# Optimization experiments

Hardware: AMD Instinct MI355X
Metric: run time of the kernel (lower is better)

The kernel has to match this reference:

```python
import jax, jax.numpy as jnp
import numpy as np
from jax.scipy.special import logsumexp

N_ALPHA = 8192
N_BETA = 8192
N_LAYERS = 16


def setup_inputs() -> dict:
    key = jax.random.key(0)
    k1, k2, k3 = jax.random.split(key, 3)
    alpha = jax.random.uniform(k1, (N_ALPHA,), jnp.float32, 1e-3, 1.0)
    alpha = alpha / alpha.sum()
    beta = jax.random.uniform(k2, (N_BETA,), jnp.float32, 1e-3, 1.0)
    beta = beta / beta.sum()
    C = jax.random.uniform(k3, (N_ALPHA, N_BETA), jnp.float32, 0.0, 1.0)
    eps = jnp.float32(0.1)
    return {"alpha": alpha, "beta": beta, "C": C, "eps": eps}


def reference(alpha, beta, C, eps):
    # Log-domain Sinkhorn iterations (tol=None -> run all n_layers).
    log_alpha = jnp.log(alpha)
    log_beta = jnp.log(beta)

    def step(carry, _):
        _, g = carry
        # log_dot_exp(C, g, eps): logsumexp over n_beta axis of (-C + g[None,:]) / eps
        f = eps * (log_alpha - logsumexp((g[None, :] - C) / eps, axis=-1))
        # log_dot_exp(C.T, f, eps): logsumexp over n_alpha axis of (-C + f[:,None]) / eps
        g_new = eps * (log_beta - logsumexp((f[:, None] - C) / eps, axis=0))
        return (f, g_new), None

    init = (jnp.zeros_like(alpha), jnp.zeros_like(beta))
    (f, g), _ = jax.lax.scan(step, init, None, length=N_LAYERS)
    return f, g
```

## Files before the change

kernel.cpp:

```cpp
#include <hip/hip_runtime.h>

#define NA 8192
#define NB 8192
#define N_LAYERS 16

typedef _Float16 half_t;
typedef _Float16 half8_t __attribute__((ext_vector_type(8)));
typedef float float4_t __attribute__((ext_vector_type(4)));

__device__ __forceinline__ void barrier_lds() {
    asm volatile("s_waitcnt lgkmcnt(0)" ::: "memory");
    __builtin_amdgcn_s_barrier();
    asm volatile("" ::: "memory");
}

template <bool READ_C, bool WRITE_E, bool HAS_V>
__global__ __launch_bounds__(256, 2) void sink_fused(
    const float* __restrict__ C, const half_t* __restrict__ Ein,
    half_t* __restrict__ Eout, const float* __restrict__ v,
    const float* __restrict__ alpha, const float* __restrict__ d_eps,
    float* __restrict__ u, float* __restrict__ partial, int n_groups)
{
    const int t = threadIdx.x;
    const int rc = blockIdx.x;
    const int row0 = rc * (n_groups * 2);
    __shared__ float sred[2][8];

    float4_t w0[4], w1[4];
    if constexpr (HAS_V) {
        const float4_t* vv = (const float4_t*)v;
#pragma unroll
        for (int k = 0; k < 4; ++k) {
            const int g = k * 256 + t;
            w0[k] = vv[2 * g];
            w1[k] = vv[2 * g + 1];
        }
    }

    float acc[4][8];
#pragma unroll
    for (int k = 0; k < 4; ++k)
#pragma unroll
        for (int j = 0; j < 8; ++j) acc[k][j] = 0.0f;

    auto usum = [&](float rs0, float rs1, int par) -> float2 {
#pragma unroll
        for (int m = 1; m < 64; m <<= 1) {
            rs0 += __shfl_xor(rs0, m, 64);
            rs1 += __shfl_xor(rs1, m, 64);
        }
        const int lane = t & 63, wid = t >> 6;
        if (lane == 0) { sred[par][wid * 2] = rs0; sred[par][wid * 2 + 1] = rs1; }
        barrier_lds();
        const float S0 = (sred[par][0] + sred[par][2]) + (sred[par][4] + sred[par][6]);
        const float S1 = (sred[par][1] + sred[par][3]) + (sred[par][5] + sred[par][7]);
        return make_float2(S0, S1);
    };

    if constexpr (!READ_C) {
        const half8_t* Eb = (const half8_t*)Ein;
        half8_t bufA[2][4], bufB[2][4];

        auto load = [&](half8_t (&d)[2][4], int r0) {
#pragma unroll
            for (int rr = 0; rr < 2; ++rr)
#pragma unroll
                for (int k = 0; k < 4; ++k)
                    d[rr][k] = Eb[(size_t)(r0 + rr) * (NB / 8) + k * 256 + t];
        };

        auto step = [&](half8_t (&cur)[2][4], half8_t (&nxt)[2][4], int r0,
                        int par, bool pf) {
            if (pf) load(nxt, r0 + 2);
            const float a0 = alpha[r0], a1 = alpha[r0 + 1];
            float rs0 = 0.0f, rs1 = 0.0f;
#pragma unroll
            for (int k = 0; k < 4; ++k) {
                rs0 += (float)cur[0][k][0] * w0[k].x + (float)cur[0][k][1] * w0[k].y +
                       (float)cur[0][k][2] * w0[k].z + (float)cur[0][k][3] * w0[k].w +
                       (float)cur[0][k][4] * w1[k].x + (float)cur[0][k][5] * w1[k].y +
                       (float)cur[0][k][6] * w1[k].z + (float)cur[0][k][7] * w1[k].w;
                rs1 += (float)cur[1][k][0] * w0[k].x + (float)cur[1][k][1] * w0[k].y +
                       (float)cur[1][k][2] * w0[k].z + (float)cur[1][k][3] * w0[k].w +
                       (float)cur[1][k][4] * w1[k].x + (float)cur[1][k][5] * w1[k].y +
                       (float)cur[1][k][6] * w1[k].z + (float)cur[1][k][7] * w1[k].w;
            }
            const float2 S = usum(rs0, rs1, par);
            const float u0 = a0 / S.x, u1 = a1 / S.y;
            if (t == 0) { u[r0] = u0; u[r0 + 1] = u1; }
#pragma unroll
            for (int k = 0; k < 4; ++k)
#pragma unroll
                for (int j = 0; j < 8; ++j)
                    acc[k][j] += u0 * (float)cur[0][k][j] + u1 * (float)cur[1][k][j];
        };

        load(bufA, row0);
        for (int s = 0; s < n_groups; s += 2) {
            step(bufA, bufB, row0 + 2 * s, 0, true);
            step(bufB, bufA, row0 + 2 * (s + 1), 1, s + 2 < n_groups);
        }
    } else {
        const float inv_eps = 1.0f / d_eps[0];
        const float4_t* Cb = (const float4_t*)C;
        float4_t bufA[2][8], bufB[2][8];

        auto load = [&](float4_t (&d)[2][8], int r0) {
#pragma unroll
            for (int rr = 0; rr < 2; ++rr)
#pragma unroll
                for (int k = 0; k < 4; ++k) {
                    const int g = k * 256 + t;
                    d[rr][2 * k]     = Cb[(size_t)(r0 + rr) * (NB / 4) + 2 * g];
                    d[rr][2 * k + 1] = Cb[(size_t)(r0 + rr) * (NB / 4) + 2 * g + 1];
                }
        };

        auto step = [&](float4_t (&cur)[2][8], float4_t (&nxt)[2][8], int r0,
                        int par, bool pf) {
            if (pf) load(nxt, r0 + 2);
            const float a0 = alpha[r0], a1 = alpha[r0 + 1];
            half8_t h[2][4];
            float rs0 = 0.0f, rs1 = 0.0f;
#pragma unroll
            for (int rr = 0; rr < 2; ++rr) {
                float rs = 0.0f;
#pragma unroll
                for (int k = 0; k < 4; ++k) {
                    const float4_t c0 = cur[rr][2 * k], c1 = cur[rr][2 * k + 1];
                    const float e0 = __expf(-c0.x * inv_eps);
                    const float e1 = __expf(-c0.y * inv_eps);
                    const float e2 = __expf(-c0.z * inv_eps);
                    const float e3 = __expf(-c0.w * inv_eps);
                    const float e4 = __expf(-c1.x * inv_eps);
                    const float e5 = __expf(-c1.y * inv_eps);
                    const float e6 = __expf(-c1.z * inv_eps);
                    const float e7 = __expf(-c1.w * inv_eps);
                    h[rr][k][0] = (_Float16)e0; h[rr][k][1] = (_Float16)e1;
                    h[rr][k][2] = (_Float16)e2; h[rr][k][3] = (_Float16)e3;
                    h[rr][k][4] = (_Float16)e4; h[rr][k][5] = (_Float16)e5;
                    h[rr][k][6] = (_Float16)e6; h[rr][k][7] = (_Float16)e7;
                    if constexpr (HAS_V) {
                        rs += e0 * w0[k].x + e1 * w0[k].y + e2 * w0[k].z + e3 * w0[k].w +
                              e4 * w1[k].x + e5 * w1[k].y + e6 * w1[k].z + e7 * w1[k].w;
                    } else {
                        rs += ((e0 + e1) + (e2 + e3)) + ((e4 + e5) + (e6 + e7));
                    }
                }
                if (rr == 0) rs0 = rs; else rs1 = rs;
            }
            if constexpr (WRITE_E) {
#pragma unroll
                for (int rr = 0; rr < 2; ++rr)
#pragma unroll
                    for (int k = 0; k < 4; ++k)
                        ((half8_t*)Eout)[(size_t)(r0 + rr) * (NB / 8) + k * 256 + t] = h[rr][k];
            }
            const float2 S = usum(rs0, rs1, par);
            const float u0 = a0 / S.x, u1 = a1 / S.y;
            if (t == 0) { u[r0] = u0; u[r0 + 1] = u1; }
#pragma unroll
            for (int k = 0; k < 4; ++k)
#pragma unroll
                for (int j = 0; j < 8; ++j)
                    acc[k][j] += u0 * (float)h[0][k][j] + u1 * (float)h[1][k][j];
        };

        load(bufA, row0);
        for (int s = 0; s < n_groups; s += 2) {
            step(bufA, bufB, row0 + 2 * s, 0, true);
            step(bufB, bufA, row0 + 2 * (s + 1), 1, s + 2 < n_groups);
        }
    }

#pragma unroll
    for (int k = 0; k < 4; ++k) {
        float4_t o0 = {acc[k][0], acc[k][1], acc[k][2], acc[k][3]};
        float4_t o1 = {acc[k][4], acc[k][5], acc[k][6], acc[k][7]};
        float4_t* p = (float4_t*)(partial + (size_t)rc * NB + (size_t)(k * 256 + t) * 8);
        p[0] = o0;
        p[1] = o1;
    }
}

__global__ __launch_bounds__(256) void sink_v_combine(
    const float* __restrict__ partial, const float* __restrict__ beta,
    float* __restrict__ v, int nvc)
{
    const int c = blockIdx.x * 32 + (threadIdx.x & 31);
    const int sl = threadIdx.x >> 5;
    float s = 0.0f;
#pragma unroll 4
    for (int i = sl; i < nvc; i += 8) s += partial[(size_t)i * NB + c];
    __shared__ float sm[8][32];
    sm[sl][threadIdx.x & 31] = s;
    __syncthreads();
    if (threadIdx.x < 32) {
        float tot = 0.0f;
#pragma unroll
        for (int k = 0; k < 8; ++k) tot += sm[k][threadIdx.x];
        v[c] = beta[c] / tot;
    }
}

__global__ __launch_bounds__(256) void sink_finalize(
    const float* __restrict__ u, const float* __restrict__ v,
    const float* __restrict__ d_eps, float* __restrict__ out)
{
    const int i = blockIdx.x * 256 + threadIdx.x;
    const float eps = d_eps[0];
    if (i < NA) {
        out[i] = eps * logf(u[i]);
    } else if (i < NA + NB) {
        out[i] = eps * logf(v[i - NA]);
    }
}

extern "C" void kernel_launch(void* const* d_in, const int* in_sizes, int n_in,
                              void* d_out, int out_size, void* d_ws, size_t ws_size,
                              hipStream_t stream)
{
    const float* alpha = (const float*)d_in[0];
    const float* beta  = (const float*)d_in[1];
    const float* C     = (const float*)d_in[2];
    const float* d_eps = (const float*)d_in[3];
    float* out = (float*)d_out;

    const size_t eBytes   = (size_t)NA * NB * sizeof(half_t);
    const size_t vecBytes = (size_t)NA * sizeof(float);

    int nvc = 0;
    bool useE = false;
    if      (ws_size >= eBytes + (size_t)512 * NB * 4 + 2 * vecBytes) { useE = true; nvc = 512; }
    else if (ws_size >= eBytes + (size_t)256 * NB * 4 + 2 * vecBytes) { useE = true; nvc = 256; }
    else if (ws_size >= eBytes + (size_t)128 * NB * 4 + 2 * vecBytes) { useE = true; nvc = 128; }
    else if (ws_size >= (size_t)512 * NB * 4 + 2 * vecBytes)          { nvc = 512; }
    else if (ws_size >= (size_t)256 * NB * 4 + 2 * vecBytes)          { nvc = 256; }
    else                                                              { nvc = 128; }

    char* ws = (char*)d_ws;
    size_t off = 0;
    half_t* E = nullptr;
    if (useE) { E = (half_t*)ws; off += eBytes; }
    float* partial = (float*)(ws + off); off += (size_t)nvc * NB * sizeof(float);
    float* u = (float*)(ws + off); off += vecBytes;
    float* v = (float*)(ws + off);

    const int ng = (NA / nvc) / 2;
    const dim3 blk(256);
    const dim3 gridF(nvc);
    const dim3 gridC(NB / 32);
    const dim3 gridFin((NA + NB) / 256);

    for (int layer = 0; layer < N_LAYERS; ++layer) {
        if (layer == 0) {
            if (useE)
                sink_fused<true, true, false><<<gridF, blk, 0, stream>>>(
                    C, nullptr, E, nullptr, alpha, d_eps, u, partial, ng);
            else
                sink_fused<true, false, false><<<gridF, blk, 0, stream>>>(
                    C, nullptr, nullptr, nullptr, alpha, d_eps, u, partial, ng);
        } else {
            if (useE)
                sink_fused<false, false, true><<<gridF, blk, 0, stream>>>(
                    nullptr, E, nullptr, v, alpha, d_eps, u, partial, ng);
            else
                sink_fused<true, false, true><<<gridF, blk, 0, stream>>>(
                    C, nullptr, nullptr, v, alpha, d_eps, u, partial, ng);
        }
        sink_v_combine<<<gridC, blk, 0, stream>>>(partial, beta, v, nvc);
    }
    sink_finalize<<<gridFin, blk, 0, stream>>>(u, v, d_eps, out);
}
```

Baseline: 1.111 ms.

## Cache partial fp16 exp(-C/eps) rows and recompute the rest from C

Replaces the all-or-nothing fp16 E cache with a partial one: each block caches as many of its 16 rows as workspace allows and recomputes the remaining rows from C with exp. Blocks become 512 threads and always number 512, with separate layer-0 and later-layer kernels. This lets the E-cache path run when the workspace cannot hold the full matrix, at the cost of extra exp work and reading fp32 C for the uncached rows. The non-cached tail has no prefetch double-buffering.

```diff
diff --git a/kernel.cpp b/kernel.cpp
--- a/kernel.cpp
+++ b/kernel.cpp
@@ -3,6 +3,9 @@
 #define NA 8192
 #define NB 8192
 #define N_LAYERS 16
+#define RPB 16
+#define NBLK 512
+#define NTH 512
 
 typedef _Float16 half_t;
 typedef _Float16 half8_t __attribute__((ext_vector_type(8)));
@@ -14,34 +17,34 @@
     asm volatile("" ::: "memory");
 }
 
-template <bool READ_C, bool WRITE_E, bool HAS_V>
-__global__ __launch_bounds__(256, 2) void sink_fused(
-    const float* __restrict__ C, const half_t* __restrict__ Ein,
-    half_t* __restrict__ Eout, const float* __restrict__ v,
-    const float* __restrict__ alpha, const float* __restrict__ d_eps,
-    float* __restrict__ u, float* __restrict__ partial, int n_groups)
+__global__ __launch_bounds__(NTH, 4) void sink_fe(
+    const half_t* __restrict__ E, const float* __restrict__ C,
+    const float* __restrict__ v, const float* __restrict__ alpha,
+    const float* __restrict__ d_eps, float* __restrict__ u,
+    float* __restrict__ partial, int ngE)
 {
     const int t = threadIdx.x;
     const int rc = blockIdx.x;
-    const int row0 = rc * (n_groups * 2);
-    __shared__ float sred[2][8];
-
-    float4_t w0[4], w1[4];
-    if constexpr (HAS_V) {
-        const float4_t* vv = (const float4_t*)v;
-#pragma unroll
-        for (int k = 0; k < 4; ++k) {
-            const int g = k * 256 + t;
-            w0[k] = vv[2 * g];
-            w1[k] = vv[2 * g + 1];
-        }
-    }
-
-    float acc[4][8];
-#pragma unroll
-    for (int k = 0; k < 4; ++k)
+    const int row0 = rc * RPB;
+    __shared__ float sred[2][16];
+
+    const float4_t* vv = (const float4_t*)v;
+    float4_t w[4];
+#pragma unroll
+    for (int k = 0; k < 2; ++k) {
+        w[2 * k]     = vv[(size_t)(k * NTH + t) * 2];
+        w[2 * k + 1] = vv[(size_t)(k * NTH + t) * 2 + 1];
+    }
+
+    float acc[2][8];
+#pragma unroll
+    for (int k = 0; k < 2; ++k)
 #pragma unroll
         for (int j = 0; j < 8; ++j) acc[k][j] = 0.0f;
+
+    const half8_t* Eb = (const half8_t*)E + (size_t)rc * (2 * ngE) * (NB / 8);
+    const float4_t* Cb = (const float4_t*)C;
+    const float inv_eps = 1.0f / d_eps[0];
 
     auto usum = [&](float rs0, float rs1, int par) -> float2 {
 #pragma unroll
@@ -52,146 +55,231 @@
         const int lane = t & 63, wid = t >> 6;
         if (lane == 0) { sred[par][wid * 2] = rs0; sred[par][wid * 2 + 1] = rs1; }
         barrier_lds();
-        const float S0 = (sred[par][0] + sred[par][2]) + (sred[par][4] + sred[par][6]);
-        const float S1 = (sred[par][1] + sred[par][3]) + (sred[par][5] + sred[par][7]);
+        float S0 = 0.0f, S1 = 0.0f;
+#pragma unroll
+        for (int q = 0; q < 8; ++q) { S0 += sred[par][q * 2]; S1 += sred[par][q * 2 + 1]; }
         return make_float2(S0, S1);
     };
 
-    if constexpr (!READ_C) {
-        const half8_t* Eb = (const half8_t*)Ein;
-        half8_t bufA[2][4], bufB[2][4];
-
-        auto load = [&](half8_t (&d)[2][4], int r0) {
-#pragma unroll
-            for (int rr = 0; rr < 2; ++rr)
-#pragma unroll
-                for (int k = 0; k < 4; ++k)
-                    d[rr][k] = Eb[(size_t)(r0 + rr) * (NB / 8) + k * 256 + t];
-        };
-
-        auto step = [&](half8_t (&cur)[2][4], half8_t (&nxt)[2][4], int r0,
-                        int par, bool pf) {
-            if (pf) load(nxt, r0 + 2);
-            const float a0 = alpha[r0], a1 = alpha[r0 + 1];
-            float rs0 = 0.0f, rs1 = 0.0f;
-#pragma unroll
-            for (int k = 0; k < 4; ++k) {
-                rs0 += (float)cur[0][k][0] * w0[k].x + (float)cur[0][k][1] * w0[k].y +
-                       (float)cur[0][k][2] * w0[k].z + (float)cur[0][k][3] * w0[k].w +
-                       (float)cur[0][k][4] * w1[k].x + (float)cur[0][k][5] * w1[k].y +
-                       (float)cur[0][k][6] * w1[k].z + (float)cur[0][k][7] * w1[k].w;
-                rs1 += (float)cur[1][k][0] * w0[k].x + (float)cur[1][k][1] * w0[k].y +
-                       (float)cur[1][k][2] * w0[k].z + (float)cur[1][k][3] * w0[k].w +
-                       (float)cur[1][k][4] * w1[k].x + (float)cur[1][k][5] * w1[k].y +
-                       (float)cur[1][k][6] * w1[k].z + (float)cur[1][k][7] * w1[k].w;
-            }
-            const float2 S = usum(rs0, rs1, par);
-            const float u0 = a0 / S.x, u1 = a1 / S.y;
-            if (t == 0) { u[r0] = u0; u[r0 + 1] = u1; }
-#pragma unroll
-            for (int k = 0; k < 4; ++k)
-#pragma unroll
-                for (int j = 0; j < 8; ++j)
-                    acc[k][j] += u0 * (float)cur[0][k][j] + u1 * (float)cur[1][k][j];
-        };
-
-        load(bufA, row0);
-        for (int s = 0; s < n_groups; s += 2) {
-            step(bufA, bufB, row0 + 2 * s, 0, true);
-            step(bufB, bufA, row0 + 2 * (s + 1), 1, s + 2 < n_groups);
-        }
-    } else {
-        const float inv_eps = 1.0f / d_eps[0];
-        const float4_t* Cb = (const float4_t*)C;
-        float4_t bufA[2][8], bufB[2][8];
-
-        auto load = [&](float4_t (&d)[2][8], int r0) {
-#pragma unroll
-            for (int rr = 0; rr < 2; ++rr)
-#pragma unroll
-                for (int k = 0; k < 4; ++k) {
-                    const int g = k * 256 + t;
-                    d[rr][2 * k]     = Cb[(size_t)(r0 + rr) * (NB / 4) + 2 * g];
-                    d[rr][2 * k + 1] = Cb[(size_t)(r0 + rr) * (NB / 4) + 2 * g + 1];
-                }
-        };
-
-        auto step = [&](float4_t (&cur)[2][8], float4_t (&nxt)[2][8], int r0,
-                        int par, bool pf) {
-            if (pf) load(nxt, r0 + 2);
-            const float a0 = alpha[r0], a1 = alpha[r0 + 1];
-            half8_t h[2][4];
-            float rs0 = 0.0f, rs1 = 0.0f;
-#pragma unroll
-            for (int rr = 0; rr < 2; ++rr) {
-                float rs = 0.0f;
-#pragma unroll
-                for (int k = 0; k < 4; ++k) {
-                    const float4_t c0 = cur[rr][2 * k], c1 = cur[rr][2 * k + 1];
-                    const float e0 = __expf(-c0.x * inv_eps);
-                    const float e1 = __expf(-c0.y * inv_eps);
-                    const float e2 = __expf(-c0.z * inv_eps);
-                    const float e3 = __expf(-c0.w * inv_eps);
-                    const float e4 = __expf(-c1.x * inv_eps);
-                    const float e5 = __expf(-c1.y * inv_eps);
-                    const float e6 = __expf(-c1.z * inv_eps);
-                    const float e7 = __expf(-c1.w * inv_eps);
-                    h[rr][k][0] = (_Float16)e0; h[rr][k][1] = (_Float16)e1;
-                    h[rr][k][2] = (_Float16)e2; h[rr][k][3] = (_Float16)e3;
-                    h[rr][k][4] = (_Float16)e4; h[rr][k][5] = (_Float16)e5;
-                    h[rr][k][6] = (_Float16)e6; h[rr][k][7] = (_Float16)e7;
-                    if constexpr (HAS_V) {
-                        rs += e0 * w0[k].x + e1 * w0[k].y + e2 * w0[k].z + e3 * w0[k].w +
-                              e4 * w1[k].x + e5 * w1[k].y + e6 * w1[k].z + e7 * w1[k].w;
-                    } else {
-                        rs += ((e0 + e1) + (e2 + e3)) + ((e4 + e5) + (e6 + e7));
-                    }
-                }
-                if (rr == 0) rs0 = rs; else rs1 = rs;
-            }
-            if constexpr (WRITE_E) {
-#pragma unroll
-                for (int rr = 0; rr < 2; ++rr)
-#pragma unroll
-                    for (int k = 0; k < 4; ++k)
-                        ((half8_t*)Eout)[(size_t)(r0 + rr) * (NB / 8) + k * 256 + t] = h[rr][k];
-            }
-            const float2 S = usum(rs0, rs1, par);
-            const float u0 = a0 / S.x, u1 = a1 / S.y;
-            if (t == 0) { u[r0] = u0; u[r0 + 1] = u1; }
-#pragma unroll
-            for (int k = 0; k < 4; ++k)
-#pragma unroll
-                for (int j = 0; j < 8; ++j)
-                    acc[k][j] += u0 * (float)h[0][k][j] + u1 * (float)h[1][k][j];
-        };
-
-        load(bufA, row0);
-        for (int s = 0; s < n_groups; s += 2) {
-            step(bufA, bufB, row0 + 2 * s, 0, true);
-            step(bufB, bufA, row0 + 2 * (s + 1), 1, s + 2 < n_groups);
-        }
-    }
-
-#pragma unroll
-    for (int k = 0; k < 4; ++k) {
+    auto dotrow = [&](const half8_t (&h)[2]) -> float {
+        float s = 0.0f;
+#pragma unroll
+        for (int k = 0; k < 2; ++k) {
+            s += (float)h[k][0] * w[2 * k].x + (float)h[k][1] * w[2 * k].y +
+                 (float)h[k][2] * w[2 * k].z + (float)h[k][3] * w[2 * k].w +
+                 (float)h[k][4] * w[2 * k + 1].x + (float)h[k][5] * w[2 * k + 1].y +
+                 (float)h[k][6] * w[2 * k + 1].z + (float)h[k][7] * w[2 * k + 1].w;
+        }
+        return s;
+    };
+
+    auto accrow = [&](float uu, const half8_t (&h)[2]) {
+#pragma unroll
+        for (int k = 0; k < 2; ++k)
+#pragma unroll
+            for (int j = 0; j < 8; ++j) acc[k][j] += uu * (float)h[k][j];
+    };
+
+    auto finish = [&](float rs0, float rs1, int g, const half8_t (&h0)[2],
+                      const half8_t (&h1)[2]) {
+        const int r0 = row0 + 2 * g;
+        const float a0 = alpha[r0], a1 = alpha[r0 + 1];
+        const float2 S = usum(rs0, rs1, g & 1);
+        const float u0 = a0 / S.x, u1 = a1 / S.y;
+        if (t == 0) { u[r0] = u0; u[r0 + 1] = u1; }
+        accrow(u0, h0);
+        accrow(u1, h1);
+    };
+
+    auto loadE = [&](half8_t (&d)[2][2], int g) {
+#pragma unroll
+        for (int rr = 0; rr < 2; ++rr)
+#pragma unroll
+            for (int k = 0; k < 2; ++k)
+                d[rr][k] = Eb[(size_t)(2 * g + rr) * (NB / 8) + k * NTH + t];
+    };
+
+    auto stepE = [&](half8_t (&cur)[2][2], half8_t (&nxt)[2][2], int g, bool pf) {
+        if (pf) loadE(nxt, g + 1);
+        const float rs0 = dotrow(cur[0]);
+        const float rs1 = dotrow(cur[1]);
+        finish(rs0, rs1, g, cur[0], cur[1]);
+    };
+
+    half8_t bufA[2][2], bufB[2][2];
+    if (ngE > 0) {
+        loadE(bufA, 0);
+        int g = 0;
+        while (g + 2 <= ngE) {
+            stepE(bufA, bufB, g, g + 1 < ngE);
+            stepE(bufB, bufA, g + 1, g + 2 < ngE);
+            g += 2;
+        }
+        if (g < ngE) stepE(bufA, bufB, g, false);
+    }
+
+    for (int g = ngE; g < RPB / 2; ++g) {
+        float4_t c[2][4];
+#pragma unroll
+        for (int rr = 0; rr < 2; ++rr)
+#pragma unroll
+            for (int k = 0; k < 2; ++k) {
+                const size_t fi = (size_t)(row0 + 2 * g + rr) * (NB / 4) +
+                                  (size_t)(k * NTH + t) * 2;
+                c[rr][2 * k]     = Cb[fi];
+                c[rr][2 * k + 1] = Cb[fi + 1];
+            }
+        half8_t h[2][2];
+#pragma unroll
+        for (int rr = 0; rr < 2; ++rr)
+#pragma unroll
+            for (int k = 0; k < 2; ++k) {
+                const float4_t ca = c[rr][2 * k], cb = c[rr][2 * k + 1];
+                h[rr][k][0] = (_Float16)__expf(-ca.x * inv_eps);
+                h[rr][k][1] = (_Float16)__expf(-ca.y * inv_eps);
+                h[rr][k][2] = (_Float16)__expf(-ca.z * inv_eps);
+                h[rr][k][3] = (_Float16)__expf(-ca.w * inv_eps);
+                h[rr][k][4] = (_Float16)__expf(-cb.x * inv_eps);
+                h[rr][k][5] = (_Float16)__expf(-cb.y * inv_eps);
+                h[rr][k][6] = (_Float16)__expf(-cb.z * inv_eps);
+                h[rr][k][7] = (_Float16)__expf(-cb.w * inv_eps);
+            }
+        const float rs0 = dotrow(h[0]);
+        const float rs1 = dotrow(h[1]);
+        finish(rs0, rs1, g, h[0], h[1]);
+    }
+
+#pragma unroll
+    for (int k = 0; k < 2; ++k) {
         float4_t o0 = {acc[k][0], acc[k][1], acc[k][2], acc[k][3]};
         float4_t o1 = {acc[k][4], acc[k][5], acc[k][6], acc[k][7]};
-        float4_t* p = (float4_t*)(partial + (size_t)rc * NB + (size_t)(k * 256 + t) * 8);
+        float4_t* p = (float4_t*)(partial + (size_t)rc * NB +
+                                  (size_t)(k * NTH + t) * 8);
         p[0] = o0;
         p[1] = o1;
     }
 }
 
+__global__ __launch_bounds__(NTH, 2) void sink_l0(
+    const float* __restrict__ C, half_t* __restrict__ E,
+    const float* __restrict__ alpha, const float* __restrict__ d_eps,
+    float* __restrict__ u, float* __restrict__ partial, int ngE)
+{
+    const int t = threadIdx.x;
+    const int rc = blockIdx.x;
+    const int row0 = rc * RPB;
+    __shared__ float sred[2][16];
+    const float inv_eps = 1.0f / d_eps[0];
+    const float4_t* Cb = (const float4_t*)C;
+    half8_t* Eh = (half8_t*)E;
+
+    float acc[2][8];
+#pragma unroll
+    for (int k = 0; k < 2; ++k)
+#pragma unroll
+        for (int j = 0; j < 8; ++j) acc[k][j] = 0.0f;
+
+    auto usum = [&](float rs0, float rs1, int par) -> float2 {
+#pragma unroll
+        for (int m = 1; m < 64; m <<= 1) {
+            rs0 += __shfl_xor(rs0, m, 64);
+            rs1 += __shfl_xor(rs1, m, 64);
+        }
+        const int lane = t & 63, wid = t >> 6;
+        if (lane == 0) { sred[par][wid * 2] = rs0; sred[par][wid * 2 + 1] = rs1; }
+        barrier_lds();
+        float S0 = 0.0f, S1 = 0.0f;
+#pragma unroll
+        for (int q = 0; q < 8; ++q) { S0 += sred[par][q * 2]; S1 += sred[par][q * 2 + 1]; }
+        return make_float2(S0, S1);
+    };
+
+    auto loadC = [&](float4_t (&d)[2][4], int g) {
+#pragma unroll
+        for (int rr = 0; rr < 2; ++rr)
+#pragma unroll
+            for (int k = 0; k < 2; ++k) {
+                const size_t fi = (size_t)(row0 + 2 * g + rr) * (NB / 4) +
+                                  (size_t)(k * NTH + t) * 2;
+                d[rr][2 * k]     = Cb[fi];
+                d[rr][2 * k + 1] = Cb[fi + 1];
+            }
+    };
+
+    auto stepC = [&](float4_t (&cur)[2][4], float4_t (&nxt)[2][4], int g, bool pf) {
+        if (pf) loadC(nxt, g + 1);
+        half8_t h[2][2];
+        float rs[2];
+#pragma unroll
+        for (int rr = 0; rr < 2; ++rr) {
+            float s = 0.0f;
+#pragma unroll
+            for (int k = 0; k < 2; ++k) {
+                const float4_t ca = cur[rr][2 * k], cb = cur[rr][2 * k + 1];
+                const float e0 = __expf(-ca.x * inv_eps);
+                const float e1 = __expf(-ca.y * inv_eps);
+                const float e2 = __expf(-ca.z * inv_eps);
+                const float e3 = __expf(-ca.w * inv_eps);
+                const float e4 = __expf(-cb.x * inv_eps);
+                const float e5 = __expf(-cb.y * inv_eps);
+                const float e6 = __expf(-cb.z * inv_eps);
+                const float e7 = __expf(-cb.w * inv_eps);
+                h[rr][k][0] = (_Float16)e0; h[rr][k][1] = (_Float16)e1;
+                h[rr][k][2] = (_Float16)e2; h[rr][k][3] = (_Float16)e3;
+                h[rr][k][4] = (_Float16)e4; h[rr][k][5] = (_Float16)e5;
+                h[rr][k][6] = (_Float16)e6; h[rr][k][7] = (_Float16)e7;
+                s += ((e0 + e1) + (e2 + e3)) + ((e4 + e5) + (e6 + e7));
+            }
+            rs[rr] = s;
+        }
+        if (g < ngE) {
+#pragma unroll
+            for (int rr = 0; rr < 2; ++rr)
+#pragma unroll
+                for (int k = 0; k < 2; ++k)
+                    Eh[(size_t)(rc * 2 * ngE + 2 * g + rr) * (NB / 8) + k * NTH + t] = h[rr][k];
+        }
+        const int r0 = row0 + 2 * g;
+        const float a0 = alpha[r0], a1 = alpha[r0 + 1];
+        const float2 S = usum(rs[0], rs[1], g & 1);
+        const float u0 = a0 / S.x, u1 = a1 / S.y;
+        if (t == 0) { u[r0] = u0; u[r0 + 1] = u1; }
+#pragma unroll
+        for (int k = 0; k < 2; ++k)
+#pragma unroll
+            for (int j = 0; j < 8; ++j) {
+                acc[k][j] += u0 * (float)h[0][k][j] + u1 * (float)h[1][k][j];
+            }
+    };
+
+    float4_t bufA[2][4], bufB[2][4];
+    loadC(bufA, 0);
+#pragma unroll
+    for (int g = 0; g < RPB / 2; g += 2) {
+        stepC(bufA, bufB, g, true);
+        stepC(bufB, bufA, g + 1, g + 2 < RPB / 2);
+    }
+
+#pragma unroll
+    for (int k = 0; k < 2; ++k) {
+        float4_t o0 = {acc[k][0], acc[k][1], acc[k][2], acc[k][3]};
+        float4_t o1 = {acc[k][4], acc[k][5], acc[k][6], acc[k][7]};
+        float4_t* p = (float4_t*)(partial + (size_t)rc * NB +
+                                  (size_t)(k * NTH + t) * 8);
+        p[0] = o0;
+        p[1] = o1;
+    }
+}
+
 __global__ __launch_bounds__(256) void sink_v_combine(
     const float* __restrict__ partial, const float* __restrict__ beta,
-    float* __restrict__ v, int nvc)
+    float* __restrict__ v)
 {
     const int c = blockIdx.x * 32 + (threadIdx.x & 31);
     const int sl = threadIdx.x >> 5;
     float s = 0.0f;
 #pragma unroll 4
-    for (int i = sl; i < nvc; i += 8) s += partial[(size_t)i * NB + c];
+    for (int i = sl; i < NBLK; i += 8) s += partial[(size_t)i * NB + c];
     __shared__ float sm[8][32];
     sm[sl][threadIdx.x & 31] = s;
     __syncthreads();
@@ -226,49 +314,40 @@
     const float* d_eps = (const float*)d_in[3];
     float* out = (float*)d_out;
 
-    const size_t eBytes   = (size_t)NA * NB * sizeof(half_t);
+    const size_t partialBytes = (size_t)NBLK * NB * sizeof(float);
     const size_t vecBytes = (size_t)NA * sizeof(float);
-
-    int nvc = 0;
-    bool useE = false;
-    if      (ws_size >= eBytes + (size_t)512 * NB * 4 + 2 * vecBytes) { useE = true; nvc = 512; }
-    else if (ws_size >= eBytes + (size_t)256 * NB * 4 + 2 * vecBytes) { useE = true; nvc = 256; }
-    else if (ws_size >= eBytes + (size_t)128 * NB * 4 + 2 * vecBytes) { useE = true; nvc = 128; }
-    else if (ws_size >= (size_t)512 * NB * 4 + 2 * vecBytes)          { nvc = 512; }
-    else if (ws_size >= (size_t)256 * NB * 4 + 2 * vecBytes)          { nvc = 256; }
-    else                                                              { nvc = 128; }
+    const size_t perK = (size_t)NBLK * NB * sizeof(half_t) / RPB * RPB;
+    const size_t kInc = (size_t)NBLK * NB * sizeof(half_t) / 8;
+    (void)perK;
+
+    size_t avail = 0;
+    if (ws_size > partialBytes + 2 * vecBytes)
+        avail = ws_size - partialBytes - 2 * vecBytes;
+    int K = (int)(avail / ((size_t)NBLK * NB * sizeof(half_t) / RPB));
+    (void)kInc;
+    if (K > RPB) K = RPB;
+    K &= ~1;
+    const int ngE = K / 2;
 
     char* ws = (char*)d_ws;
     size_t off = 0;
-    half_t* E = nullptr;
-    if (useE) { E = (half_t*)ws; off += eBytes; }
-    float* partial = (float*)(ws + off); off += (size_t)nvc * NB * sizeof(float);
+    half_t* E = (half_t*)ws;
+    off += (size_t)NBLK * K * NB * sizeof(half_t);
+    float* partial = (float*)(ws + off); off += partialBytes;
     float* u = (float*)(ws + off); off += vecBytes;
     float* v = (float*)(ws + off);
 
-    const int ng = (NA / nvc) / 2;
-    const dim3 blk(256);
-    const dim3 gridF(nvc);
+    const dim3 blkF(NTH), blkS(256);
+    const dim3 gridF(NBLK);
     const dim3 gridC(NB / 32);
     const dim3 gridFin((NA + NB) / 256);
 
     for (int layer = 0; layer < N_LAYERS; ++layer) {
-        if (layer == 0) {
-            if (useE)
-                sink_fused<true, true, false><<<gridF, blk, 0, stream>>>(
-                    C, nullptr, E, nullptr, alpha, d_eps, u, partial, ng);
-            else
-                sink_fused<true, false, false><<<gridF, blk, 0, stream>>>(
-                    C, nullptr, nullptr, nullptr, alpha, d_eps, u, partial, ng);
-        } else {
-            if (useE)
-                sink_fused<false, false, true><<<gridF, blk, 0, stream>>>(
-                    nullptr, E, nullptr, v, alpha, d_eps, u, partial, ng);
-            else
-                sink_fused<true, false, true><<<gridF, blk, 0, stream>>>(
-                    C, nullptr, nullptr, v, alpha, d_eps, u, partial, ng);
-        }
-        sink_v_combine<<<gridC, blk, 0, stream>>>(partial, beta, v, nvc);
-    }
-    sink_finalize<<<gridFin, blk, 0, stream>>>(u, v, d_eps, out);
-}
+        if (layer == 0)
+            sink_l0<<<gridF, blkF, 0, stream>>>(C, E, alpha, d_eps, u, partial, ngE);
+        else
+            sink_fe<<<gridF, blkF, 0, stream>>>(E, C, v, alpha, d_eps, u, partial, ngE);
+        sink_v_combine<<<gridC, blkS, 0, stream>>>(partial, beta, v);
+    }
+    sink_finalize<<<gridFin, blkS, 0, stream>>>(u, v, d_eps, out);
+}
```

New measurement: 2.375 ms. +113.9%, slower.

## Restructure Sinkhorn kernels to 512-thread blocks with 4-row episodes and partial E cache

Applied to the files above, without the earlier changes.

Replaces the templated fused kernel with three specialized kernels using 512 threads per block, 16 rows per block, and four rows reduced per barrier episode instead of two. This halves the number of block-wide barriers per row and widens per-thread work. It also adds a partial-cache mode, where only as many fp16 E rows as fit in the workspace are stored and the rest are recomputed from C. The cost is higher register pressure from four buffered rows, and the fixed 512-block partial buffer.

```diff
diff --git a/kernel.cpp b/kernel.cpp
--- a/kernel.cpp
+++ b/kernel.cpp
@@ -3,6 +3,9 @@
 #define NA 8192
 #define NB 8192
 #define N_LAYERS 16
+#define RPB 16
+#define NBLK 512
+#define NTH 512
 
 typedef _Float16 half_t;
 typedef _Float16 half8_t __attribute__((ext_vector_type(8)));
@@ -14,184 +17,338 @@
     asm volatile("" ::: "memory");
 }
 
-template <bool READ_C, bool WRITE_E, bool HAS_V>
-__global__ __launch_bounds__(256, 2) void sink_fused(
-    const float* __restrict__ C, const half_t* __restrict__ Ein,
-    half_t* __restrict__ Eout, const float* __restrict__ v,
-    const float* __restrict__ alpha, const float* __restrict__ d_eps,
-    float* __restrict__ u, float* __restrict__ partial, int n_groups)
+__global__ __launch_bounds__(NTH, 4) void sink_fe_full(
+    const half_t* __restrict__ E, const float* __restrict__ v,
+    const float* __restrict__ alpha, float* __restrict__ u,
+    float* __restrict__ partial)
 {
     const int t = threadIdx.x;
     const int rc = blockIdx.x;
-    const int row0 = rc * (n_groups * 2);
-    __shared__ float sred[2][8];
-
-    float4_t w0[4], w1[4];
-    if constexpr (HAS_V) {
-        const float4_t* vv = (const float4_t*)v;
-#pragma unroll
-        for (int k = 0; k < 4; ++k) {
-            const int g = k * 256 + t;
-            w0[k] = vv[2 * g];
-            w1[k] = vv[2 * g + 1];
-        }
-    }
-
-    float acc[4][8];
-#pragma unroll
-    for (int k = 0; k < 4; ++k)
-#pragma unroll
-        for (int j = 0; j < 8; ++j) acc[k][j] = 0.0f;
-
-    auto usum = [&](float rs0, float rs1, int par) -> float2 {
+    const int row0 = rc * RPB;
+    __shared__ float4_t sred[2][8];
+
+    const float4_t* vv = (const float4_t*)v;
+    const float4_t wA0 = vv[2 * t], wA1 = vv[2 * t + 1];
+    const float4_t wB0 = vv[1024 + 2 * t], wB1 = vv[1024 + 2 * t + 1];
+
+    float acc[16];
+#pragma unroll
+    for (int j = 0; j < 16; ++j) acc[j] = 0.0f;
+
+    const half8_t* Eb = (const half8_t*)E;
+    const size_t rbase = (size_t)row0 * (NB / 8);
+
+    half8_t eC[4][2], eN[4][2];
+    auto loadB = [&](half8_t (&d)[4][2], int b) {
+#pragma unroll
+        for (int r = 0; r < 4; ++r) {
+            const size_t ro = rbase + (size_t)(b * 4 + r) * (NB / 8);
+            d[r][0] = Eb[ro + t];
+            d[r][1] = Eb[ro + 512 + t];
+        }
+    };
+
+    auto episode = [&](const half8_t (&e)[4][2], int b, int par) {
+        float rs0, rs1, rs2, rs3;
+        {
+            float s[4];
+#pragma unroll
+            for (int r = 0; r < 4; ++r) {
+                float x = 0.0f;
+                x += (float)e[r][0][0] * wA0.x + (float)e[r][0][1] * wA0.y +
+                     (float)e[r][0][2] * wA0.z + (float)e[r][0][3] * wA0.w;
+                x += (float)e[r][0][4] * wA1.x + (float)e[r][0][5] * wA1.y +
+                     (float)e[r][0][6] * wA1.z + (float)e[r][0][7] * wA1.w;
+                x += (float)e[r][1][0] * wB0.x + (float)e[r][1][1] * wB0.y +
+                     (float)e[r][1][2] * wB0.z + (float)e[r][1][3] * wB0.w;
+                x += (float)e[r][1][4] * wB1.x + (float)e[r][1][5] * wB1.y +
+                     (float)e[r][1][6] * wB1.z + (float)e[r][1][7] * wB1.w;
+                s[r] = x;
+            }
+            rs0 = s[0]; rs1 = s[1]; rs2 = s[2]; rs3 = s[3];
+        }
 #pragma unroll
         for (int m = 1; m < 64; m <<= 1) {
-            rs0 += __shfl_xor(rs0, m, 64);
-            rs1 += __shfl_xor(rs1, m, 64);
-        }
-        const int lane = t & 63, wid = t >> 6;
-        if (lane == 0) { sred[par][wid * 2] = rs0; sred[par][wid * 2 + 1] = rs1; }
+            rs0 += __shfl_xor(rs0, m);
+            rs1 += __shfl_xor(rs1, m);
+            rs2 += __shfl_xor(rs2, m);
+            rs3 += __shfl_xor(rs3, m);
+        }
+        if ((t & 63) == 0) sred[par][t >> 6] = float4_t{rs0, rs1, rs2, rs3};
         barrier_lds();
-        const float S0 = (sred[par][0] + sred[par][2]) + (sred[par][4] + sred[par][6]);
-        const float S1 = (sred[par][1] + sred[par][3]) + (sred[par][5] + sred[par][7]);
-        return make_float2(S0, S1);
+        float4_t S = sred[par][0];
+#pragma unroll
+        for (int w2 = 1; w2 < 8; ++w2) S += sred[par][w2];
+
+        const int r0 = row0 + b * 4;
+        const float u0 = alpha[r0] / S.x;
+        const float u1 = alpha[r0 + 1] / S.y;
+        const float u2 = alpha[r0 + 2] / S.z;
+        const float u3 = alpha[r0 + 3] / S.w;
+        if (t == 0) *(float4_t*)(u + r0) = float4_t{u0, u1, u2, u3};
+
+#pragma unroll
+        for (int j = 0; j < 8; ++j) {
+            acc[j]     += u0 * (float)e[0][0][j] + u1 * (float)e[1][0][j] +
+                          u2 * (float)e[2][0][j] + u3 * (float)e[3][0][j];
+            acc[8 + j] += u0 * (float)e[0][1][j] + u1 * (float)e[1][1][j] +
+                          u2 * (float)e[2][1][j] + u3 * (float)e[3][1][j];
+        }
     };
 
-    if constexpr (!READ_C) {
-        const half8_t* Eb = (const half8_t*)Ein;
-        half8_t bufA[2][4], bufB[2][4];
-
-        auto load = [&](half8_t (&d)[2][4], int r0) {
-#pragma unroll
-            for (int rr = 0; rr < 2; ++rr)
-#pragma unroll
-                for (int k = 0; k < 4; ++k)
-                    d[rr][k] = Eb[(size_t)(r0 + rr) * (NB / 8) + k * 256 + t];
-        };
-
-        auto step = [&](half8_t (&cur)[2][4], half8_t (&nxt)[2][4], int r0,
-                        int par, bool pf) {
-            if (pf) load(nxt, r0 + 2);
-            const float a0 = alpha[r0], a1 = alpha[r0 + 1];
-            float rs0 = 0.0f, rs1 = 0.0f;
-#pragma unroll
-            for (int k = 0; k < 4; ++k) {
-                rs0 += (float)cur[0][k][0] * w0[k].x + (float)cur[0][k][1] * w0[k].y +
-                       (float)cur[0][k][2] * w0[k].z + (float)cur[0][k][3] * w0[k].w +
-                       (float)cur[0][k][4] * w1[k].x + (float)cur[0][k][5] * w1[k].y +
-                       (float)cur[0][k][6] * w1[k].z + (float)cur[0][k][7] * w1[k].w;
-                rs1 += (float)cur[1][k][0] * w0[k].x + (float)cur[1][k][1] * w0[k].y +
-                       (float)cur[1][k][2] * w0[k].z + (float)cur[1][k][3] * w0[k].w +
-                       (float)cur[1][k][4] * w1[k].x + (float)cur[1][k][5] * w1[k].y +
-                       (float)cur[1][k][6] * w1[k].z + (float)cur[1][k][7] * w1[k].w;
+    loadB(eC, 0);
+    loadB(eN, 1);
+    episode(eC, 0, 0);
+    loadB(eC, 2);
+    episode(eN, 1, 1);
+    loadB(eN, 3);
+    episode(eC, 2, 0);
+    episode(eN, 3, 1);
+
+    float* pr = partial + (size_t)rc * NB;
+    *(float4_t*)(pr + 8 * t)        = float4_t{acc[0], acc[1], acc[2], acc[3]};
+    *(float4_t*)(pr + 8 * t + 4)    = float4_t{acc[4], acc[5], acc[6], acc[7]};
+    *(float4_t*)(pr + 4096 + 8 * t)     = float4_t{acc[8], acc[9], acc[10], acc[11]};
+    *(float4_t*)(pr + 4096 + 8 * t + 4) = float4_t{acc[12], acc[13], acc[14], acc[15]};
+}
+
+__global__ __launch_bounds__(NTH, 4) void sink_l0(
+    const float* __restrict__ C, half_t* __restrict__ E,
+    const float* __restrict__ alpha, const float* __restrict__ d_eps,
+    float* __restrict__ u, float* __restrict__ partial, int KC)
+{
+    const int t = threadIdx.x;
+    const int rc = blockIdx.x;
+    const int row0 = rc * RPB;
+    const float inv_eps = 1.0f / d_eps[0];
+    __shared__ float4_t sred[2][8];
+
+    float acc[16];
+#pragma unroll
+    for (int j = 0; j < 16; ++j) acc[j] = 0.0f;
+
+    const float4_t* Cb = (const float4_t*)C;
+    half8_t* Eh = (half8_t*)E;
+
+    float4_t cA[4], cB[4];
+    auto loadRow = [&](float4_t (&d)[4], int lr) {
+        const size_t ro = (size_t)(row0 + lr) * (NB / 4);
+        d[0] = Cb[ro + 2 * t];
+        d[1] = Cb[ro + 2 * t + 1];
+        d[2] = Cb[ro + 1024 + 2 * t];
+        d[3] = Cb[ro + 1024 + 2 * t + 1];
+    };
+
+    half8_t h[4][2];
+    float rs[4];
+
+    auto procRow = [&](const float4_t (&c)[4], int b, int r, int lr) {
+        half8_t h0, h1;
+        float s = 0.0f;
+        {
+            const float e0 = __expf(-c[0].x * inv_eps);
+            const float e1 = __expf(-c[0].y * inv_eps);
+            const float e2 = __expf(-c[0].z * inv_eps);
+            const float e3 = __expf(-c[0].w * inv_eps);
+            const float e4 = __expf(-c[1].x * inv_eps);
+            const float e5 = __expf(-c[1].y * inv_eps);
+            const float e6 = __expf(-c[1].z * inv_eps);
+            const float e7 = __expf(-c[1].w * inv_eps);
+            h0[0] = (_Float16)e0; h0[1] = (_Float16)e1; h0[2] = (_Float16)e2;
+            h0[3] = (_Float16)e3; h0[4] = (_Float16)e4; h0[5] = (_Float16)e5;
+            h0[6] = (_Float16)e6; h0[7] = (_Float16)e7;
+            s += ((e0 + e1) + (e2 + e3)) + ((e4 + e5) + (e6 + e7));
+        }
+        {
+            const float e0 = __expf(-c[2].x * inv_eps);
+            const float e1 = __expf(-c[2].y * inv_eps);
+            const float e2 = __expf(-c[2].z * inv_eps);
+            const float e3 = __expf(-c[2].w * inv_eps);
+            const float e4 = __expf(-c[3].x * inv_eps);
+            const float e5 = __expf(-c[3].y * inv_eps);
+            const float e6 = __expf(-c[3].z * inv_eps);
+            const float e7 = __expf(-c[3].w * inv_eps);
+            h1[0] = (_Float16)e0; h1[1] = (_Float16)e1; h1[2] = (_Float16)e2;
+            h1[3] = (_Float16)e3; h1[4] = (_Float16)e4; h1[5] = (_Float16)e5;
+            h1[6] = (_Float16)e6; h1[7] = (_Float16)e7;
+            s += ((e0 + e1) + (e2 + e3)) + ((e4 + e5) + (e6 + e7));
+        }
+        h[r][0] = h0;
+        h[r][1] = h1;
+        rs[r] = s;
+        if (lr < KC) {
+            const size_t eo = (size_t)(rc * KC + lr) * (NB / 8);
+            Eh[eo + t] = h0;
+            Eh[eo + 512 + t] = h1;
+        }
+    };
+
+    auto episode = [&](int b, int par) {
+        float rs0 = rs[0], rs1 = rs[1], rs2 = rs[2], rs3 = rs[3];
+#pragma unroll
+        for (int m = 1; m < 64; m <<= 1) {
+            rs0 += __shfl_xor(rs0, m);
+            rs1 += __shfl_xor(rs1, m);
+            rs2 += __shfl_xor(rs2, m);
+            rs3 += __shfl_xor(rs3, m);
+        }
+        if ((t & 63) == 0) sred[par][t >> 6] = float4_t{rs0, rs1, rs2, rs3};
+        barrier_lds();
+        float4_t S = sred[par][0];
+#pragma unroll
+        for (int w2 = 1; w2 < 8; ++w2) S += sred[par][w2];
+        const int r0 = row0 + b * 4;
+        const float u0 = alpha[r0] / S.x;
+        const float u1 = alpha[r0 + 1] / S.y;
+        const float u2 = alpha[r0 + 2] / S.z;
+        const float u3 = alpha[r0 + 3] / S.w;
+        if (t == 0) *(float4_t*)(u + r0) = float4_t{u0, u1, u2, u3};
+#pragma unroll
+        for (int j = 0; j < 8; ++j) {
+            acc[j]     += u0 * (float)h[0][0][j] + u1 * (float)h[1][0][j] +
+                          u2 * (float)h[2][0][j] + u3 * (float)h[3][0][j];
+            acc[8 + j] += u0 * (float)h[0][1][j] + u1 * (float)h[1][1][j] +
+                          u2 * (float)h[2][1][j] + u3 * (float)h[3][1][j];
+        }
+    };
+
+    loadRow(cA, 0);
+#pragma unroll
+    for (int b = 0; b < 4; ++b) {
+#pragma unroll
+        for (int r = 0; r < 4; ++r) {
+            const int lr = b * 4 + r;
+            if (lr & 1) {
+                if (lr < RPB - 1) loadRow(cA, lr + 1);
+                procRow(cB, b, r, lr);
+            } else {
+                if (lr < RPB - 1) loadRow(cB, lr + 1);
+                procRow(cA, b, r, lr);
             }
-            const float2 S = usum(rs0, rs1, par);
-            const float u0 = a0 / S.x, u1 = a1 / S.y;
-            if (t == 0) { u[r0] = u0; u[r0 + 1] = u1; }
-#pragma unroll
-            for (int k = 0; k < 4; ++k)
-#pragma unroll
-                for (int j = 0; j < 8; ++j)
-                    acc[k][j] += u0 * (float)cur[0][k][j] + u1 * (float)cur[1][k][j];
-        };
-
-        load(bufA, row0);
-        for (int s = 0; s < n_groups; s += 2) {
-            step(bufA, bufB, row0 + 2 * s, 0, true);
-            step(bufB, bufA, row0 + 2 * (s + 1), 1, s + 2 < n_groups);
-        }
-    } else {
-        const float inv_eps = 1.0f / d_eps[0];
-        const float4_t* Cb = (const float4_t*)C;
-        float4_t bufA[2][8], bufB[2][8];
-
-        auto load = [&](float4_t (&d)[2][8], int r0) {
-#pragma unroll
-            for (int rr = 0; rr < 2; ++rr)
-#pragma unroll
-                for (int k = 0; k < 4; ++k) {
-                    const int g = k * 256 + t;
-                    d[rr][2 * k]     = Cb[(size_t)(r0 + rr) * (NB / 4) + 2 * g];
-                    d[rr][2 * k + 1] = Cb[(size_t)(r0 + rr) * (NB / 4) + 2 * g + 1];
-                }
-        };
-
-        auto step = [&](float4_t (&cur)[2][8], float4_t (&nxt)[2][8], int r0,
-                        int par, bool pf) {
-            if (pf) load(nxt, r0 + 2);
-            const float a0 = alpha[r0], a1 = alpha[r0 + 1];
-            half8_t h[2][4];
-            float rs0 = 0.0f, rs1 = 0.0f;
-#pragma unroll
-            for (int rr = 0; rr < 2; ++rr) {
-                float rs = 0.0f;
-#pragma unroll
-                for (int k = 0; k < 4; ++k) {
-                    const float4_t c0 = cur[rr][2 * k], c1 = cur[rr][2 * k + 1];
-                    const float e0 = __expf(-c0.x * inv_eps);
-                    const float e1 = __expf(-c0.y * inv_eps);
-                    const float e2 = __expf(-c0.z * inv_eps);
-                    const float e3 = __expf(-c0.w * inv_eps);
-                    const float e4 = __expf(-c1.x * inv_eps);
-                    const float e5 = __expf(-c1.y * inv_eps);
-                    const float e6 = __expf(-c1.z * inv_eps);
-                    const float e7 = __expf(-c1.w * inv_eps);
-                    h[rr][k][0] = (_Float16)e0; h[rr][k][1] = (_Float16)e1;
-                    h[rr][k][2] = (_Float16)e2; h[rr][k][3] = (_Float16)e3;
-                    h[rr][k][4] = (_Float16)e4; h[rr][k][5] = (_Float16)e5;
-                    h[rr][k][6] = (_Float16)e6; h[rr][k][7] = (_Float16)e7;
-                    if constexpr (HAS_V) {
-                        rs += e0 * w0[k].x + e1 * w0[k].y + e2 * w0[k].z + e3 * w0[k].w +
-                              e4 * w1[k].x + e5 * w1[k].y + e6 * w1[k].z + e7 * w1[k].w;
-                    } else {
-                        rs += ((e0 + e1) + (e2 + e3)) + ((e4 + e5) + (e6 + e7));
-                    }
-                }
-                if (rr == 0) rs0 = rs; else rs1 = rs;
+        }
+        episode(b, b & 1);
+    }
+
+    float* pr = partial + (size_t)rc * NB;
+    *(float4_t*)(pr + 8 * t)        = float4_t{acc[0], acc[1], acc[2], acc[3]};
+    *(float4_t*)(pr + 8 * t + 4)    = float4_t{acc[4], acc[5], acc[6], acc[7]};
+    *(float4_t*)(pr + 4096 + 8 * t)     = float4_t{acc[8], acc[9], acc[10], acc[11]};
+    *(float4_t*)(pr + 4096 + 8 * t + 4) = float4_t{acc[12], acc[13], acc[14], acc[15]};
+}
+
+__global__ __launch_bounds__(NTH, 4) void sink_fe_part(
+    const half_t* __restrict__ E, const float* __restrict__ C,
+    const float* __restrict__ v, const float* __restrict__ alpha,
+    const float* __restrict__ d_eps, float* __restrict__ u,
+    float* __restrict__ partial, int KC)
+{
+    const int t = threadIdx.x;
+    const int rc = blockIdx.x;
+    const int row0 = rc * RPB;
+    const float inv_eps = 1.0f / d_eps[0];
+    __shared__ float4_t sred[2][8];
+
+    const float4_t* vv = (const float4_t*)v;
+    const float4_t wA0 = vv[2 * t], wA1 = vv[2 * t + 1];
+    const float4_t wB0 = vv[1024 + 2 * t], wB1 = vv[1024 + 2 * t + 1];
+
+    float acc[16];
+#pragma unroll
+    for (int j = 0; j < 16; ++j) acc[j] = 0.0f;
+
+    const half8_t* Eb = (const half8_t*)E;
+    const float4_t* Cb = (const float4_t*)C;
+    half8_t h[4][2];
+    float rs[4];
+
+    for (int b = 0; b < 4; ++b) {
+#pragma unroll
+        for (int r = 0; r < 4; ++r) {
+            const int lr = b * 4 + r;
+            half8_t h0, h1;
+            if (lr < KC) {
+                const size_t eo = (size_t)(rc * KC + lr) * (NB / 8);
+                h0 = Eb[eo + t];
+                h1 = Eb[eo + 512 + t];
+            } else {
+                const size_t ro = (size_t)(row0 + lr) * (NB / 4);
+                const float4_t c0 = Cb[ro + 2 * t], c1 = Cb[ro + 2 * t + 1];
+                const float4_t c2 = Cb[ro + 1024 + 2 * t], c3 = Cb[ro + 1024 + 2 * t + 1];
+                h0[0] = (_Float16)__expf(-c0.x * inv_eps);
+                h0[1] = (_Float16)__expf(-c0.y * inv_eps);
+                h0[2] = (_Float16)__expf(-c0.z * inv_eps);
+                h0[3] = (_Float16)__expf(-c0.w * inv_eps);
+                h0[4] = (_Float16)__expf(-c1.x * inv_eps);
+                h0[5] = (_Float16)__expf(-c1.y * inv_eps);
+                h0[6] = (_Float16)__expf(-c1.z * inv_eps);
+                h0[7] = (_Float16)__expf(-c1.w * inv_eps);
+                h1[0] = (_Float16)__expf(-c2.x * inv_eps);
+                h1[1] = (_Float16)__expf(-c2.y * inv_eps);
+                h1[2] = (_Float16)__expf(-c2.z * inv_eps);
+                h1[3] = (_Float16)__expf(-c2.w * inv_eps);
+                h1[4] = (_Float16)__expf(-c3.x * inv_eps);
+                h1[5] = (_Float16)__expf(-c3.y * inv_eps);
+                h1[6] = (_Float16)__expf(-c3.z * inv_eps);
+                h1[7] = (_Float16)__expf(-c3.w * inv_eps);
             }
-            if constexpr (WRITE_E) {
-#pragma unroll
-                for (int rr = 0; rr < 2; ++rr)
-#pragma unroll
-                    for (int k = 0; k < 4; ++k)
-                        ((half8_t*)Eout)[(size_t)(r0 + rr) * (NB / 8) + k * 256 + t] = h[rr][k];
-            }
-            const float2 S = usum(rs0, rs1, par);
-            const float u0 = a0 / S.x, u1 = a1 / S.y;
-            if (t == 0) { u[r0] = u0; u[r0 + 1] = u1; }
-#pragma unroll
-            for (int k = 0; k < 4; ++k)
-#pragma unroll
-                for (int j = 0; j < 8; ++j)
-                    acc[k][j] += u0 * (float)h[0][k][j] + u1 * (float)h[1][k][j];
-        };
-
-        load(bufA, row0);
-        for (int s = 0; s < n_groups; s += 2) {
-            step(bufA, bufB, row0 + 2 * s, 0, true);
-            step(bufB, bufA, row0 + 2 * (s + 1), 1, s + 2 < n_groups);
-        }
-    }
-
-#pragma unroll
-    for (int k = 0; k < 4; ++k) {
-        float4_t o0 = {acc[k][0], acc[k][1], acc[k][2], acc[k][3]};
-        float4_t o1 = {acc[k][4], acc[k][5], acc[k][6], acc[k][7]};
-        float4_t* p = (float4_t*)(partial + (size_t)rc * NB + (size_t)(k * 256 + t) * 8);
-        p[0] = o0;
-        p[1] = o1;
-    }
+            h[r][0] = h0;
+            h[r][1] = h1;
+            float x = 0.0f;
+            x += (float)h0[0] * wA0.x + (float)h0[1] * wA0.y +
+                 (float)h0[2] * wA0.z + (float)h0[3] * wA0.w;
+            x += (float)h0[4] * wA1.x + (float)h0[5] * wA1.y +
+                 (float)h0[6] * wA1.z + (float)h0[7] * wA1.w;
+            x += (float)h1[0] * wB0.x + (float)h1[1] * wB0.y +
+                 (float)h1[2] * wB0.z + (float)h1[3] * wB0.w;
+            x += (float)h1[4] * wB1.x + (float)h1[5] * wB1.y +
+                 (float)h1[6] * wB1.z + (float)h1[7] * wB1.w;
+            rs[r] = x;
+        }
+        float rs0 = rs[0], rs1 = rs[1], rs2 = rs[2], rs3 = rs[3];
+#pragma unroll
+        for (int m = 1; m < 64; m <<= 1) {
+            rs0 += __shfl_xor(rs0, m);
+            rs1 += __shfl_xor(rs1, m);
+            rs2 += __shfl_xor(rs2, m);
+            rs3 += __shfl_xor(rs3, m);
+        }
+        const int par = b & 1;
+        if ((t & 63) == 0) sred[par][t >> 6] = float4_t{rs0, rs1, rs2, rs3};
+        barrier_lds();
+        float4_t S = sred[par][0];
+#pragma unroll
+        for (int w2 = 1; w2 < 8; ++w2) S += sred[par][w2];
+        const int r0 = row0 + b * 4;
+        const float u0 = alpha[r0] / S.x;
+        const float u1 = alpha[r0 + 1] / S.y;
+        const float u2 = alpha[r0 + 2] / S.z;
+        const float u3 = alpha[r0 + 3] / S.w;
+        if (t == 0) *(float4_t*)(u + r0) = float4_t{u0, u1, u2, u3};
+#pragma unroll
+        for (int j = 0; j < 8; ++j) {
+            acc[j]     += u0 * (float)h[0][0][j] + u1 * (float)h[1][0][j] +
+                          u2 * (float)h[2][0][j] + u3 * (float)h[3][0][j];
+            acc[8 + j] += u0 * (float)h[0][1][j] + u1 * (float)h[1][1][j] +
+                          u2 * (float)h[2][1][j] + u3 * (float)h[3][1][j];
+        }
+    }
+
+    float* pr = partial + (size_t)rc * NB;
+    *(float4_t*)(pr + 8 * t)        = float4_t{acc[0], acc[1], acc[2], acc[3]};
+    *(float4_t*)(pr + 8 * t + 4)    = float4_t{acc[4], acc[5], acc[6], acc[7]};
+    *(float4_t*)(pr + 4096 + 8 * t)     = float4_t{acc[8], acc[9], acc[10], acc[11]};
+    *(float4_t*)(pr + 4096 + 8 * t + 4) = float4_t{acc[12], acc[13], acc[14], acc[15]};
 }
 
 __global__ __launch_bounds__(256) void sink_v_combine(
     const float* __restrict__ partial, const float* __restrict__ beta,
-    float* __restrict__ v, int nvc)
+    float* __restrict__ v)
 {
     const int c = blockIdx.x * 32 + (threadIdx.x & 31);
     const int sl = threadIdx.x >> 5;
     float s = 0.0f;
 #pragma unroll 4
-    for (int i = sl; i < nvc; i += 8) s += partial[(size_t)i * NB + c];
+    for (int i = sl; i < NBLK; i += 8) s += partial[(size_t)i * NB + c];
     __shared__ float sm[8][32];
     sm[sl][threadIdx.x & 31] = s;
     __syncthreads();
@@ -226,49 +383,43 @@
     const float* d_eps = (const float*)d_in[3];
     float* out = (float*)d_out;
 
-    const size_t eBytes   = (size_t)NA * NB * sizeof(half_t);
-    const size_t vecBytes = (size_t)NA * sizeof(float);
-
-    int nvc = 0;
-    bool useE = false;
-    if      (ws_size >= eBytes + (size_t)512 * NB * 4 + 2 * vecBytes) { useE = true; nvc = 512; }
-    else if (ws_size >= eBytes + (size_t)256 * NB * 4 + 2 * vecBytes) { useE = true; nvc = 256; }
-    else if (ws_size >= eBytes + (size_t)128 * NB * 4 + 2 * vecBytes) { useE = true; nvc = 128; }
-    else if (ws_size >= (size_t)512 * NB * 4 + 2 * vecBytes)          { nvc = 512; }
-    else if (ws_size >= (size_t)256 * NB * 4 + 2 * vecBytes)          { nvc = 256; }
-    else                                                              { nvc = 128; }
+    const size_t pB   = (size_t)NBLK * NB * sizeof(float);
+    const size_t vecB = (size_t)NA * sizeof(float);
+    const size_t perK = (size_t)NBLK * NB * sizeof(half_t);
+    const size_t eFull = perK * RPB;
+
+    int KC = RPB;
+    {
+        size_t avail = (ws_size > pB + 2 * vecB) ? ws_size - pB - 2 * vecB : 0;
+        if (avail < eFull) {
+            KC = (int)(avail / perK);
+            if (KC > RPB) KC = RPB;
+            KC &= ~1;
+        }
+    }
 
     char* ws = (char*)d_ws;
     size_t off = 0;
-    half_t* E = nullptr;
-    if (useE) { E = (half_t*)ws; off += eBytes; }
-    float* partial = (float*)(ws + off); off += (size_t)nvc * NB * sizeof(float);
-    float* u = (float*)(ws + off); off += vecBytes;
+    half_t* E = (half_t*)ws; off += perK * KC;
+    float* partial = (float*)(ws + off); off += pB;
+    float* u = (float*)(ws + off); off += vecB;
     float* v = (float*)(ws + off);
 
-    const int ng = (NA / nvc) / 2;
-    const dim3 blk(256);
-    const dim3 gridF(nvc);
+    const dim3 blkF(NTH), blkS(256);
+    const dim3 gridF(NBLK);
     const dim3 gridC(NB / 32);
     const dim3 gridFin((NA + NB) / 256);
 
     for (int layer = 0; layer < N_LAYERS; ++layer) {
         if (layer == 0) {
-            if (useE)
-                sink_fused<true, true, false><<<gridF, blk, 0, stream>>>(
-                    C, nullptr, E, nullptr, alpha, d_eps, u, partial, ng);
-            else
-                sink_fused<true, false, false><<<gridF, blk, 0, stream>>>(
-                    C, nullptr, nullptr, nullptr, alpha, d_eps, u, partial, ng);
+            sink_l0<<<gridF, blkF, 0, stream>>>(C, E, alpha, d_eps, u, partial, KC);
+        } else if (KC == RPB) {
+            sink_fe_full<<<gridF, blkF, 0, stream>>>(E, v, alpha, u, partial);
         } else {
-            if (useE)
-                sink_fused<false, false, true><<<gridF, blk, 0, stream>>>(
-                    nullptr, E, nullptr, v, alpha, d_eps, u, partial, ng);
-            else
-                sink_fused<true, false, true><<<gridF, blk, 0, stream>>>(
-                    C, nullptr, nullptr, v, alpha, d_eps, u, partial, ng);
-        }
-        sink_v_combine<<<gridC, blk, 0, stream>>>(partial, beta, v, nvc);
-    }
-    sink_finalize<<<gridFin, blk, 0, stream>>>(u, v, d_eps, out);
-}
+            sink_fe_part<<<gridF, blkF, 0, stream>>>(E, C, v, alpha, d_eps, u,
+                                                     partial, KC);
+        }
+        sink_v_combine<<<gridC, blkS, 0, stream>>>(partial, beta, v);
+    }
+    sink_finalize<<<gridFin, blkS, 0, stream>>>(u, v, d_eps, out);
+}
```

Measured after the change: 2.403 ms. 116% more time.
